# Optimization experiments

Measured on AMD Instinct MI355X. Metric: run time of the kernel, lower is better.

Reference implementation:

```python
import jax, jax.numpy as jnp
import numpy as np

N_PTS = 1_000_000
RES = 512
RANK = 48
OUT = 32
INIT_SCALE = 0.1


def _plane_sample(plane, gx, gy):
    """Bilinear grid_sample, align_corners=True, border padding.
    plane: [R, Res, Res] (R=rank); gx, gy: [N] in [-1,1] -> [R, N]."""
    res = plane.shape[-1]
    px = jnp.clip((gx + 1.0) * 0.5 * (res - 1), 0.0, res - 1.0)
    py = jnp.clip((gy + 1.0) * 0.5 * (res - 1), 0.0, res - 1.0)
    x0 = jnp.floor(px).astype(jnp.int32)
    y0 = jnp.floor(py).astype(jnp.int32)
    x1 = jnp.minimum(x0 + 1, res - 1)
    y1 = jnp.minimum(y0 + 1, res - 1)
    wx = px - x0.astype(px.dtype)
    wy = py - y0.astype(py.dtype)
    # gathers: [R, N] each
    v00 = plane[:, y0, x0]
    v01 = plane[:, y0, x1]
    v10 = plane[:, y1, x0]
    v11 = plane[:, y1, x1]
    return (v00 * (1 - wy) * (1 - wx) + v01 * (1 - wy) * wx
            + v10 * wy * (1 - wx) + v11 * wy * wx)


def _line_sample(line, gy):
    """Line is [R, Res] (width dim of size 1 collapses; x coord is 0 -> px=0).
    1-D linear interp along Res with gy in [-1,1] -> [R, N]."""
    res = line.shape[-1]
    py = jnp.clip((gy + 1.0) * 0.5 * (res - 1), 0.0, res - 1.0)
    y0 = jnp.floor(py).astype(jnp.int32)
    y1 = jnp.minimum(y0 + 1, res - 1)
    wy = py - y0.astype(py.dtype)
    return line[:, y0] * (1 - wy) + line[:, y1] * wy


def _geo_forward(coordinates, plane_xy, plane_xz, plane_yz,
                 line_z, line_y, line_x, proj_w, proj_b):
    coords = coordinates * 2.0 - 1.0  # [N, 3] in [-1, 1]
    cx, cy, cz = coords[:, 0], coords[:, 1], coords[:, 2]
    vm = (_plane_sample(plane_xy, cx, cy) * _line_sample(line_z, cz)
          + _plane_sample(plane_xz, cx, cz) * _line_sample(line_y, cy)
          + _plane_sample(plane_yz, cy, cz) * _line_sample(line_x, cx))  # [R, N]
    # projection: [N, R] @ [R, OUT] + b
    return vm.T @ proj_w.T + proj_b


def setup_inputs() -> dict:
    key = jax.random.key(0)
    ks = jax.random.split(key, 9)
    return {
        "coordinates": jax.random.uniform(ks[0], (N_PTS, 3), dtype=jnp.float32),
        "plane_xy": jax.random.normal(ks[1], (RANK, RES, RES), jnp.float32) * INIT_SCALE,
        "plane_xz": jax.random.normal(ks[2], (RANK, RES, RES), jnp.float32) * INIT_SCALE,
        "plane_yz": jax.random.normal(ks[3], (RANK, RES, RES), jnp.float32) * INIT_SCALE,
        "line_z": jax.random.normal(ks[4], (RANK, RES), jnp.float32) * INIT_SCALE,
        "line_y": jax.random.normal(ks[5], (RANK, RES), jnp.float32) * INIT_SCALE,
        "line_x": jax.random.normal(ks[6], (RANK, RES), jnp.float32) * INIT_SCALE,
        "proj_w": jax.random.normal(ks[7], (OUT, RANK), jnp.float32) * INIT_SCALE,
        "proj_b": jnp.zeros((OUT,), jnp.float32),
    }


def reference(coordinates, plane_xy, plane_xz, plane_yz,
              line_z, line_y, line_x, proj_w, proj_b):
    return _geo_forward(coordinates, plane_xy, plane_xz, plane_yz,
                        line_z, line_y, line_x, proj_w, proj_b)
```

## Files before the change

### kernel.cpp

```cpp
#include <hip/hip_runtime.h>
#include <stdint.h>

#define RES      512
#define TEXELS   (RES * RES)
#define NPTS     1000000
#define RANK     48
#define ODIM     32
#define PPB      64
#define VMS      52
#define OSTR     33
#define CELLS    32768
#define LINB     6
#define CNTB     256
#define TPB      1536
#define SCTB     1024

typedef unsigned int u32;
typedef float vf4 __attribute__((ext_vector_type(4)));

__device__ __forceinline__ float lobf(u32 u) { return __uint_as_float(u << 16); }
__device__ __forceinline__ float hibf(u32 u) { return __uint_as_float(u & 0xffff0000u); }

__device__ __forceinline__ float ntl(const float* p) {
    return __builtin_nontemporal_load(p);
}

__device__ __forceinline__ u32 pkbf(float a, float b) {
    u32 x = __float_as_uint(a), y = __float_as_uint(b);
    u32 xr = (x + 0x7fffu + ((x >> 16) & 1u)) >> 16;
    u32 yr = (y + 0x7fffu + ((y >> 16) & 1u)) & 0xffff0000u;
    return xr | yr;
}

__device__ __forceinline__ u32 sprd5(u32 a) {
    a &= 31u;
    a = (a | (a << 8)) & 0x100Fu;
    a = (a | (a << 4)) & 0x10C3u;
    a = (a | (a << 2)) & 0x1249u;
    return a;
}
__device__ __forceinline__ u32 cellOf(float x, float y, float z) {
    u32 cx = (u32)fminf(fmaxf(x * 32.f, 0.f), 31.f);
    u32 cy = (u32)fminf(fmaxf(y * 32.f, 0.f), 31.f);
    u32 cz = (u32)fminf(fmaxf(z * 32.f, 0.f), 31.f);
    return sprd5(cx) | (sprd5(cy) << 1) | (sprd5(cz) << 2);
}

__device__ __forceinline__ void tp_one(int g,
    const float* __restrict__ p0, const float* __restrict__ p1,
    const float* __restrict__ p2, char* __restrict__ ws)
{
    int plane = g >> 18;
    int texel = g & (TEXELS - 1);
    const float* src = (plane == 0) ? p0 : ((plane == 1) ? p1 : p2);
    u32 c2[24];
#pragma unroll
    for (int h = 0; h < 2; ++h) {
        float fa[12], fb[12];
#pragma unroll
        for (int d = 0; d < 12; ++d) {
            fa[d] = ntl(src + (size_t)(2 * (h * 12 + d) + 0) * TEXELS + texel);
            fb[d] = ntl(src + (size_t)(2 * (h * 12 + d) + 1) * TEXELS + texel);
        }
#pragma unroll
        for (int d = 0; d < 12; ++d) c2[h * 12 + d] = pkbf(fa[d], fb[d]);
    }
    char* dst = ws + (size_t)plane * TEXELS * 96 + (size_t)texel * 96;
#pragma unroll
    for (int s = 0; s < 6; ++s) {
        uint4 q = make_uint4(c2[4 * s + 0], c2[4 * s + 1],
                             c2[4 * s + 2], c2[4 * s + 3]);
        *(uint4*)(dst + 16 * s) = q;
    }
}

__device__ __forceinline__ void lines_role(int j, int t,
    const float* __restrict__ lz, const float* __restrict__ ly,
    const float* __restrict__ lx, char* __restrict__ ws)
{
    int id = j * 256 + t;
    int line = id >> 9;
    int pos = id & (RES - 1);
    const float* src = (line == 0) ? lz : ((line == 1) ? ly : lx);
    char* dst = ws + (size_t)3 * TEXELS * 96 + (size_t)line * RES * 96
                   + (size_t)pos * 96;
#pragma unroll
    for (int k = 0; k < 6; ++k) {
        uint4 q;
        q.x = pkbf(ntl(&src[(8 * k + 0) * RES + pos]), ntl(&src[(8 * k + 1) * RES + pos]));
        q.y = pkbf(ntl(&src[(8 * k + 2) * RES + pos]), ntl(&src[(8 * k + 3) * RES + pos]));
        q.z = pkbf(ntl(&src[(8 * k + 4) * RES + pos]), ntl(&src[(8 * k + 5) * RES + pos]));
        q.w = pkbf(ntl(&src[(8 * k + 6) * RES + pos]), ntl(&src[(8 * k + 7) * RES + pos]));
        *(uint4*)(dst + 16 * k) = q;
    }
}

__global__ __launch_bounds__(256) void k1_prep(
    const float* __restrict__ coords, u32* __restrict__ counts,
    const float* __restrict__ p0, const float* __restrict__ p1,
    const float* __restrict__ p2,
    const float* __restrict__ lz, const float* __restrict__ ly,
    const float* __restrict__ lx, char* __restrict__ ws)
{
    int bx = blockIdx.x, t = threadIdx.x;
    if (bx < LINB) {
        lines_role(bx, t, lz, ly, lx, ws);
    } else if (bx < LINB + CNTB) {
        for (int idx = (bx - LINB) * 256 + t; idx < NPTS; idx += CNTB * 256) {
            float x = ntl(&coords[3 * idx + 0]);
            float y = ntl(&coords[3 * idx + 1]);
            float z = ntl(&coords[3 * idx + 2]);
            atomicAdd(&counts[cellOf(x, y, z)], 1u);
        }
    } else {
        int w = bx - LINB - CNTB;
        for (int g = w * 256 + t; g < 3 * TEXELS; g += TPB * 256)
            tp_one(g, p0, p1, p2, ws);
    }
}

__global__ __launch_bounds__(1024) void k2_scan(
    const u32* __restrict__ counts, u32* __restrict__ cursors)
{
    __shared__ u32 wt[16];
    int t = threadIdx.x;
    u32 local[32];
    u32 s = 0;
#pragma unroll
    for (int i = 0; i < 32; ++i) {
        local[i] = s;
        s += counts[t * 32 + i];
    }
    u32 tot = s;
    int lane = t & 63, w = t >> 6;
    u32 incl = tot;
#pragma unroll
    for (int d = 1; d < 64; d <<= 1) {
        u32 v = __shfl_up(incl, d);
        if (lane >= d) incl += v;
    }
    if (lane == 63) wt[w] = incl;
    __syncthreads();
    if (t == 0) {
        u32 a = 0;
#pragma unroll
        for (int i = 0; i < 16; ++i) { u32 x = wt[i]; wt[i] = a; a += x; }
    }
    __syncthreads();
    u32 base = wt[w] + (incl - tot);
#pragma unroll
    for (int i = 0; i < 32; ++i)
        cursors[t * 32 + i] = base + local[i];
}

__global__ __launch_bounds__(256) void k3_scatter(
    const float* __restrict__ coords, u32* __restrict__ cursors,
    vf4* __restrict__ rc2)
{
    int t = threadIdx.x;
    for (int idx = blockIdx.x * 256 + t; idx < NPTS; idx += SCTB * 256) {
        float x = ntl(&coords[3 * idx + 0]);
        float y = ntl(&coords[3 * idx + 1]);
        float z = ntl(&coords[3 * idx + 2]);
        u32 pos = atomicAdd(&cursors[cellOf(x, y, z)], 1u);
        vf4 v; v.x = x; v.y = y; v.z = z; v.w = __uint_as_float((u32)idx);
        __builtin_nontemporal_store(v, rc2 + pos);
    }
}

__global__ __launch_bounds__(256) void tp_stream_only(
    const float* __restrict__ p0, const float* __restrict__ p1,
    const float* __restrict__ p2, char* __restrict__ ws)
{
    int g = blockIdx.x * 256 + threadIdx.x;
    tp_one(g, p0, p1, p2, ws);
}
__global__ __launch_bounds__(256) void lines_only(
    const float* __restrict__ lz, const float* __restrict__ ly,
    const float* __restrict__ lx, char* __restrict__ ws)
{
    lines_role(blockIdx.x, threadIdx.x, lz, ly, lx, ws);
}

__device__ __forceinline__ void prep1(float g, int& i0, int& i1, float& w) {
    float p = fminf(fmaxf((g + 1.f) * 0.5f * 511.f, 0.f), 511.f);
    float fp = floorf(p);
    i0 = (int)fp;
    i1 = min(i0 + 1, RES - 1);
    w = p - fp;
}

template <int TEXB, bool SORTED>
__global__ __launch_bounds__(512, 4) void geo_main(
    const void* __restrict__ cin, const char* __restrict__ ws,
    const float* __restrict__ W, const float* __restrict__ Bb,
    float* __restrict__ out)
{
    __shared__ float vm_lds[PPB * VMS];
    __shared__ u32 opt_lds[PPB];

    int tid = threadIdx.x;
    int ptL = tid >> 3;
    int c = tid & 7;

    int bid = blockIdx.x;
    if (SORTED) {
        int nwg = gridDim.x;
        int q = nwg >> 3, r = nwg & 7;
        int xcd = bid & 7, slot = bid >> 3;
        bid = (xcd < r ? xcd * (q + 1) : r * (q + 1) + (xcd - r) * q) + slot;
    }
    int pt = bid * PPB + ptL;

    float gx, gy, gz;
    if (SORTED) {
        vf4 cc = __builtin_nontemporal_load((const vf4*)cin + pt);
        gx = cc.x * 2.f - 1.f;
        gy = cc.y * 2.f - 1.f;
        gz = cc.z * 2.f - 1.f;
        if (c == 0) opt_lds[ptL] = __float_as_uint(cc.w);
    } else {
        const float* coords = (const float*)cin;
        gx = ntl(&coords[3 * pt + 0]) * 2.f - 1.f;
        gy = ntl(&coords[3 * pt + 1]) * 2.f - 1.f;
        gz = ntl(&coords[3 * pt + 2]) * 2.f - 1.f;
        if (c == 0) opt_lds[ptL] = (u32)pt;
    }

    int x0, x1, y0, y1, z0, z1;
    float wx, wy, wz;
    prep1(gx, x0, x1, wx);
    prep1(gy, y0, y1, wy);
    prep1(gz, z0, z1, wz);

    const size_t PW = (size_t)TEXELS * TEXB;
    const size_t LW = (size_t)RES * TEXB;
    const char* pxy = ws;
    const char* pxz = ws + PW;
    const char* pyz = ws + 2 * PW;
    const char* lzb = ws + 3 * PW;
    const char* lyb = lzb + LW;
    const char* lxb = lyb + LW;

    u32 co = 12u * (u32)c;

    u32 q[12][3], le[3][3], lf[3][3];
    {
        u32 offs[12];
        offs[0] = (u32)(y0 * RES + x0) * TEXB + co;
        offs[1] = (u32)(y0 * RES + x1) * TEXB + co;
        offs[2] = (u32)(y1 * RES + x0) * TEXB + co;
        offs[3] = (u32)(y1 * RES + x1) * TEXB + co;
        offs[4] = (u32)(z0 * RES + x0) * TEXB + co;
        offs[5] = (u32)(z0 * RES + x1) * TEXB + co;
        offs[6] = (u32)(z1 * RES + x0) * TEXB + co;
        offs[7] = (u32)(z1 * RES + x1) * TEXB + co;
        offs[8]  = (u32)(z0 * RES + y0) * TEXB + co;
        offs[9]  = (u32)(z0 * RES + y1) * TEXB + co;
        offs[10] = (u32)(z1 * RES + y0) * TEXB + co;
        offs[11] = (u32)(z1 * RES + y1) * TEXB + co;
        const char* bases[3] = { pxy, pxz, pyz };
#pragma unroll
        for (int p = 0; p < 3; ++p) {
#pragma unroll
            for (int k = 0; k < 4; ++k) {
                const u32* s = (const u32*)(bases[p] + offs[4 * p + k]);
                q[4 * p + k][0] = s[0];
                q[4 * p + k][1] = s[1];
                q[4 * p + k][2] = s[2];
            }
        }
        const char* lb[3] = { lzb, lyb, lxb };
        u32 l0[3] = { (u32)z0 * TEXB + co, (u32)y0 * TEXB + co, (u32)x0 * TEXB + co };
        u32 l1[3] = { (u32)z1 * TEXB + co, (u32)y1 * TEXB + co, (u32)x1 * TEXB + co };
#pragma unroll
        for (int p = 0; p < 3; ++p) {
            const u32* s0 = (const u32*)(lb[p] + l0[p]);
            const u32* s1 = (const u32*)(lb[p] + l1[p]);
            le[p][0] = s0[0]; le[p][1] = s0[1]; le[p][2] = s0[2];
            lf[p][0] = s1[0]; lf[p][1] = s1[1]; lf[p][2] = s1[2];
        }
    }

    float pw[3][4];
    pw[0][0] = (1.f - wy) * (1.f - wx); pw[0][1] = (1.f - wy) * wx;
    pw[0][2] = wy * (1.f - wx);         pw[0][3] = wy * wx;
    pw[1][0] = (1.f - wz) * (1.f - wx); pw[1][1] = (1.f - wz) * wx;
    pw[1][2] = wz * (1.f - wx);         pw[1][3] = wz * wx;
    pw[2][0] = (1.f - wz) * (1.f - wy); pw[2][1] = (1.f - wz) * wy;
    pw[2][2] = wz * (1.f - wy);         pw[2][3] = wz * wy;
    float lw[3] = { wz, wy, wx };

    float vm[6] = { 0.f, 0.f, 0.f, 0.f, 0.f, 0.f };
#pragma unroll
    for (int p = 0; p < 3; ++p) {
        float s0 = pw[p][0], s1 = pw[p][1], s2 = pw[p][2], s3 = pw[p][3];
        float il = 1.f - lw[p], wl = lw[p];
#pragma unroll
        for (int d = 0; d < 3; ++d) {
            u32 a = q[4 * p + 0][d], b = q[4 * p + 1][d];
            u32 cc = q[4 * p + 2][d], dd = q[4 * p + 3][d];
            float slo = s0 * lobf(a) + s1 * lobf(b) + s2 * lobf(cc) + s3 * lobf(dd);
            float shi = s0 * hibf(a) + s1 * hibf(b) + s2 * hibf(cc) + s3 * hibf(dd);
            float llo = il * lobf(le[p][d]) + wl * lobf(lf[p][d]);
            float lhi = il * hibf(le[p][d]) + wl * hibf(lf[p][d]);
            vm[2 * d + 0] = fmaf(slo, llo, vm[2 * d + 0]);
            vm[2 * d + 1] = fmaf(shi, lhi, vm[2 * d + 1]);
        }
    }

    float* vr = vm_lds + ptL * VMS + 6 * c;
    *(float2*)(vr + 0) = make_float2(vm[0], vm[1]);
    *(float2*)(vr + 2) = make_float2(vm[2], vm[3]);
    *(float2*)(vr + 4) = make_float2(vm[4], vm[5]);

    __syncthreads();

    int wav = __builtin_amdgcn_readfirstlane(tid >> 6);
    int lane = tid & 63;
    int ob = wav * 4;

    const float* vmrow = vm_lds + lane * VMS;
    float4 bb = *(const float4*)(Bb + ob);
    float a0 = bb.x, a1 = bb.y, a2 = bb.z, a3 = bb.w;
#pragma unroll 4
    for (int k = 0; k < 12; ++k) {
        float4 v = *(const float4*)(vmrow + 4 * k);
        float4 w0 = *(const float4*)(W + (ob + 0) * RANK + 4 * k);
        float4 w1 = *(const float4*)(W + (ob + 1) * RANK + 4 * k);
        float4 w2 = *(const float4*)(W + (ob + 2) * RANK + 4 * k);
        float4 w3 = *(const float4*)(W + (ob + 3) * RANK + 4 * k);
        a0 = fmaf(v.x, w0.x, a0); a0 = fmaf(v.y, w0.y, a0);
        a0 = fmaf(v.z, w0.z, a0); a0 = fmaf(v.w, w0.w, a0);
        a1 = fmaf(v.x, w1.x, a1); a1 = fmaf(v.y, w1.y, a1);
        a1 = fmaf(v.z, w1.z, a1); a1 = fmaf(v.w, w1.w, a1);
        a2 = fmaf(v.x, w2.x, a2); a2 = fmaf(v.y, w2.y, a2);
        a2 = fmaf(v.z, w2.z, a2); a2 = fmaf(v.w, w2.w, a2);
        a3 = fmaf(v.x, w3.x, a3); a3 = fmaf(v.y, w3.y, a3);
        a3 = fmaf(v.z, w3.z, a3); a3 = fmaf(v.w, w3.w, a3);
    }

    __syncthreads();
    {
        vf4 r; r.x = a0; r.y = a1; r.z = a2; r.w = a3;
        *(vf4*)(vm_lds + lane * OSTR + ob) = r;
    }
    __syncthreads();
    {
        int p8 = lane >> 3;
        int c2 = lane & 7;
        int gp = wav * 8 + p8;
        vf4 v = *(const vf4*)(vm_lds + gp * OSTR + 4 * c2);
        size_t orow = (size_t)opt_lds[gp];
        __builtin_nontemporal_store(v, (vf4*)(out + orow * ODIM + 4 * c2));
    }
}

extern "C" void kernel_launch(void* const* d_in, const int* in_sizes, int n_in,
                              void* d_out, int out_size, void* d_ws, size_t ws_size,
                              hipStream_t stream) {
    const float* coords = (const float*)d_in[0];
    const float* pxy = (const float*)d_in[1];
    const float* pxz = (const float*)d_in[2];
    const float* pyz = (const float*)d_in[3];
    const float* lz = (const float*)d_in[4];
    const float* ly = (const float*)d_in[5];
    const float* lx = (const float*)d_in[6];
    const float* W = (const float*)d_in[7];
    const float* Bb = (const float*)d_in[8];
    float* out = (float*)d_out;
    char* ws = (char*)d_ws;

    size_t pool96 = (size_t)3 * TEXELS * 96 + (size_t)3 * RES * 96;
    size_t o_counts = (pool96 + 255) & ~(size_t)255;
    size_t o_cursors = o_counts + (size_t)CELLS * 4;
    size_t o_rc2 = o_cursors + (size_t)CELLS * 4;
    size_t need_sorted = o_rc2 + (size_t)NPTS * 16;

    if (ws_size >= need_sorted) {
        u32* counts = (u32*)(ws + o_counts);
        u32* cursors = (u32*)(ws + o_cursors);
        vf4* rc2 = (vf4*)(ws + o_rc2);

        hipMemsetAsync(counts, 0, (size_t)CELLS * 4, stream);
        k1_prep<<<LINB + CNTB + TPB, 256, 0, stream>>>(coords, counts,
                                                       pxy, pxz, pyz,
                                                       lz, ly, lx, ws);
        k2_scan<<<1, 1024, 0, stream>>>(counts, cursors);
        k3_scatter<<<SCTB, 256, 0, stream>>>(coords, cursors, rc2);
        geo_main<96, true><<<NPTS / PPB, 512, 0, stream>>>(rc2, ws, W, Bb, out);
    } else {
        tp_stream_only<<<3 * TEXELS / 256, 256, 0, stream>>>(pxy, pxz, pyz, ws);
        lines_only<<<6, 256, 0, stream>>>(lz, ly, lx, ws);
        geo_main<96, false><<<NPTS / PPB, 512, 0, stream>>>(coords, ws, W, Bb, out);
    }
}
```

Baseline: 474.8 us.

## Use per-segment LDS histograms for binning and vectorize plane transpose

Replaces the global-atomic counting sort over a 32^3 Morton grid with a coarser 16^3 grid, where each of 256 segments builds a shared-memory histogram. A column-wise prefix over segments plus a base scan then lets the scatter kernel use LDS atomics. The memset and global atomic contention go away, and the scatter stays deterministic within each segment. The plane transpose now reads four texels per float4 load and writes four 96-byte records per thread. The coarser cells may reduce sampling locality in the main kernel.

```diff
diff --git a/kernel.cpp b/kernel.cpp
--- a/kernel.cpp
+++ b/kernel.cpp
@@ -9,11 +9,11 @@
 #define PPB      64
 #define VMS      52
 #define OSTR     33
-#define CELLS    32768
+#define NCELL    4096
+#define NSEG     256
+#define SEGSZ    3907
 #define LINB     6
-#define CNTB     256
-#define TPB      1536
-#define SCTB     1024
+#define TPB4     768
 
 typedef unsigned int u32;
 typedef float vf4 __attribute__((ext_vector_type(4)));
@@ -23,6 +23,9 @@
 
 __device__ __forceinline__ float ntl(const float* p) {
     return __builtin_nontemporal_load(p);
+}
+__device__ __forceinline__ vf4 ntl4(const float* p) {
+    return __builtin_nontemporal_load((const vf4*)p);
 }
 
 __device__ __forceinline__ u32 pkbf(float a, float b) {
@@ -32,45 +35,45 @@
     return xr | yr;
 }
 
-__device__ __forceinline__ u32 sprd5(u32 a) {
-    a &= 31u;
-    a = (a | (a << 8)) & 0x100Fu;
-    a = (a | (a << 4)) & 0x10C3u;
-    a = (a | (a << 2)) & 0x1249u;
+__device__ __forceinline__ u32 sprd4(u32 a) {
+    a &= 15u;
+    a = (a | (a << 4)) & 0x0C3u;
+    a = (a | (a << 2)) & 0x249u;
     return a;
 }
 __device__ __forceinline__ u32 cellOf(float x, float y, float z) {
-    u32 cx = (u32)fminf(fmaxf(x * 32.f, 0.f), 31.f);
-    u32 cy = (u32)fminf(fmaxf(y * 32.f, 0.f), 31.f);
-    u32 cz = (u32)fminf(fmaxf(z * 32.f, 0.f), 31.f);
-    return sprd5(cx) | (sprd5(cy) << 1) | (sprd5(cz) << 2);
-}
-
-__device__ __forceinline__ void tp_one(int g,
+    u32 cx = (u32)fminf(fmaxf(x * 16.f, 0.f), 15.f);
+    u32 cy = (u32)fminf(fmaxf(y * 16.f, 0.f), 15.f);
+    u32 cz = (u32)fminf(fmaxf(z * 16.f, 0.f), 15.f);
+    return sprd4(cx) | (sprd4(cy) << 1) | (sprd4(cz) << 2);
+}
+
+__device__ __forceinline__ void tp_one4(int g4,
     const float* __restrict__ p0, const float* __restrict__ p1,
     const float* __restrict__ p2, char* __restrict__ ws)
 {
-    int plane = g >> 18;
-    int texel = g & (TEXELS - 1);
+    int plane = g4 >> 16;
+    int t4 = g4 & (TEXELS / 4 - 1);
     const float* src = (plane == 0) ? p0 : ((plane == 1) ? p1 : p2);
-    u32 c2[24];
-#pragma unroll
-    for (int h = 0; h < 2; ++h) {
-        float fa[12], fb[12];
-#pragma unroll
-        for (int d = 0; d < 12; ++d) {
-            fa[d] = ntl(src + (size_t)(2 * (h * 12 + d) + 0) * TEXELS + texel);
-            fb[d] = ntl(src + (size_t)(2 * (h * 12 + d) + 1) * TEXELS + texel);
-        }
-#pragma unroll
-        for (int d = 0; d < 12; ++d) c2[h * 12 + d] = pkbf(fa[d], fb[d]);
-    }
-    char* dst = ws + (size_t)plane * TEXELS * 96 + (size_t)texel * 96;
+    int tex0 = t4 * 4;
+    char* dst = ws + (size_t)plane * TEXELS * 96 + (size_t)tex0 * 96;
 #pragma unroll
     for (int s = 0; s < 6; ++s) {
-        uint4 q = make_uint4(c2[4 * s + 0], c2[4 * s + 1],
-                             c2[4 * s + 2], c2[4 * s + 3]);
-        *(uint4*)(dst + 16 * s) = q;
+        vf4 fa[4], fb[4];
+#pragma unroll
+        for (int d = 0; d < 4; ++d) {
+            int dd = 4 * s + d;
+            fa[d] = ntl4(src + (size_t)(2 * dd + 0) * TEXELS + tex0);
+            fb[d] = ntl4(src + (size_t)(2 * dd + 1) * TEXELS + tex0);
+        }
+#pragma unroll
+        for (int k = 0; k < 4; ++k) {
+            uint4 q = make_uint4(pkbf(fa[0][k], fb[0][k]),
+                                 pkbf(fa[1][k], fb[1][k]),
+                                 pkbf(fa[2][k], fb[2][k]),
+                                 pkbf(fa[3][k], fb[3][k]));
+            *(uint4*)(dst + (size_t)k * 96 + 16 * s) = q;
+        }
     }
 }
 
@@ -96,41 +99,65 @@
 }
 
 __global__ __launch_bounds__(256) void k1_prep(
-    const float* __restrict__ coords, u32* __restrict__ counts,
+    const float* __restrict__ coords, u32* __restrict__ T,
     const float* __restrict__ p0, const float* __restrict__ p1,
     const float* __restrict__ p2,
     const float* __restrict__ lz, const float* __restrict__ ly,
     const float* __restrict__ lx, char* __restrict__ ws)
 {
+    __shared__ u32 hist[NCELL];
     int bx = blockIdx.x, t = threadIdx.x;
     if (bx < LINB) {
         lines_role(bx, t, lz, ly, lx, ws);
-    } else if (bx < LINB + CNTB) {
-        for (int idx = (bx - LINB) * 256 + t; idx < NPTS; idx += CNTB * 256) {
+    } else if (bx < LINB + NSEG) {
+        int s = bx - LINB;
+#pragma unroll
+        for (int i = 0; i < NCELL / 256; ++i) hist[t + 256 * i] = 0u;
+        __syncthreads();
+        int base = s * SEGSZ;
+        int lim = min(base + SEGSZ, NPTS);
+#pragma unroll 1
+        for (int idx = base + t; idx < lim; idx += 256) {
             float x = ntl(&coords[3 * idx + 0]);
             float y = ntl(&coords[3 * idx + 1]);
             float z = ntl(&coords[3 * idx + 2]);
-            atomicAdd(&counts[cellOf(x, y, z)], 1u);
+            atomicAdd(&hist[cellOf(x, y, z)], 1u);
+        }
+        __syncthreads();
+        u32* Ts = T + (size_t)s * NCELL;
+#pragma unroll
+        for (int i = 0; i < NCELL / 256; ++i) {
+            int cc = t + 256 * i;
+            Ts[cc] = hist[cc];
         }
     } else {
-        int w = bx - LINB - CNTB;
-        for (int g = w * 256 + t; g < 3 * TEXELS; g += TPB * 256)
-            tp_one(g, p0, p1, p2, ws);
-    }
-}
-
-__global__ __launch_bounds__(1024) void k2_scan(
-    const u32* __restrict__ counts, u32* __restrict__ cursors)
-{
-    __shared__ u32 wt[16];
+        tp_one4((bx - LINB - NSEG) * 256 + t, p0, p1, p2, ws);
+    }
+}
+
+__global__ __launch_bounds__(256) void k2_prefix(
+    u32* __restrict__ T, u32* __restrict__ cellTot)
+{
+    int c = blockIdx.x * 256 + threadIdx.x;
+    u32 run = 0;
+#pragma unroll 8
+    for (int s = 0; s < NSEG; ++s) {
+        u32 v = T[(size_t)s * NCELL + c];
+        T[(size_t)s * NCELL + c] = run;
+        run += v;
+    }
+    cellTot[c] = run;
+}
+
+__global__ __launch_bounds__(256) void k2_base(
+    const u32* __restrict__ cellTot, u32* __restrict__ cellBase)
+{
+    __shared__ u32 wt[4];
     int t = threadIdx.x;
-    u32 local[32];
+    u32 loc[16];
     u32 s = 0;
 #pragma unroll
-    for (int i = 0; i < 32; ++i) {
-        local[i] = s;
-        s += counts[t * 32 + i];
-    }
+    for (int i = 0; i < 16; ++i) { loc[i] = s; s += cellTot[t * 16 + i]; }
     u32 tot = s;
     int lane = t & 63, w = t >> 6;
     u32 incl = tot;
@@ -141,28 +168,34 @@
     }
     if (lane == 63) wt[w] = incl;
     __syncthreads();
-    if (t == 0) {
-        u32 a = 0;
-#pragma unroll
-        for (int i = 0; i < 16; ++i) { u32 x = wt[i]; wt[i] = a; a += x; }
+    u32 base = incl - tot;
+#pragma unroll
+    for (int i = 0; i < 4; ++i) base += (i < w) ? wt[i] : 0u;
+#pragma unroll
+    for (int i = 0; i < 16; ++i) cellBase[t * 16 + i] = base + loc[i];
+}
+
+__global__ __launch_bounds__(256) void k3_scatter(
+    const float* __restrict__ coords, const u32* __restrict__ T,
+    const u32* __restrict__ cellBase, vf4* __restrict__ rc2)
+{
+    __shared__ u32 cur[NCELL];
+    int s = blockIdx.x, t = threadIdx.x;
+    const u32* Ts = T + (size_t)s * NCELL;
+#pragma unroll
+    for (int i = 0; i < NCELL / 256; ++i) {
+        int cc = t + 256 * i;
+        cur[cc] = cellBase[cc] + Ts[cc];
     }
     __syncthreads();
-    u32 base = wt[w] + (incl - tot);
-#pragma unroll
-    for (int i = 0; i < 32; ++i)
-        cursors[t * 32 + i] = base + local[i];
-}
-
-__global__ __launch_bounds__(256) void k3_scatter(
-    const float* __restrict__ coords, u32* __restrict__ cursors,
-    vf4* __restrict__ rc2)
-{
-    int t = threadIdx.x;
-    for (int idx = blockIdx.x * 256 + t; idx < NPTS; idx += SCTB * 256) {
+    int base = s * SEGSZ;
+    int lim = min(base + SEGSZ, NPTS);
+#pragma unroll 1
+    for (int idx = base + t; idx < lim; idx += 256) {
         float x = ntl(&coords[3 * idx + 0]);
         float y = ntl(&coords[3 * idx + 1]);
         float z = ntl(&coords[3 * idx + 2]);
-        u32 pos = atomicAdd(&cursors[cellOf(x, y, z)], 1u);
+        u32 pos = atomicAdd(&cur[cellOf(x, y, z)], 1u);
         vf4 v; v.x = x; v.y = y; v.z = z; v.w = __uint_as_float((u32)idx);
         __builtin_nontemporal_store(v, rc2 + pos);
     }
@@ -172,8 +205,7 @@
     const float* __restrict__ p0, const float* __restrict__ p1,
     const float* __restrict__ p2, char* __restrict__ ws)
 {
-    int g = blockIdx.x * 256 + threadIdx.x;
-    tp_one(g, p0, p1, p2, ws);
+    tp_one4(blockIdx.x * 256 + threadIdx.x, p0, p1, p2, ws);
 }
 __global__ __launch_bounds__(256) void lines_only(
     const float* __restrict__ lz, const float* __restrict__ ly,
@@ -372,25 +404,27 @@
     char* ws = (char*)d_ws;
 
     size_t pool96 = (size_t)3 * TEXELS * 96 + (size_t)3 * RES * 96;
-    size_t o_counts = (pool96 + 255) & ~(size_t)255;
-    size_t o_cursors = o_counts + (size_t)CELLS * 4;
-    size_t o_rc2 = o_cursors + (size_t)CELLS * 4;
+    size_t o_T = (pool96 + 255) & ~(size_t)255;
+    size_t o_ct = o_T + (size_t)NSEG * NCELL * 4;
+    size_t o_cb = o_ct + (size_t)NCELL * 4;
+    size_t o_rc2 = o_cb + (size_t)NCELL * 4;
     size_t need_sorted = o_rc2 + (size_t)NPTS * 16;
 
     if (ws_size >= need_sorted) {
-        u32* counts = (u32*)(ws + o_counts);
-        u32* cursors = (u32*)(ws + o_cursors);
+        u32* T = (u32*)(ws + o_T);
+        u32* cellTot = (u32*)(ws + o_ct);
+        u32* cellBase = (u32*)(ws + o_cb);
         vf4* rc2 = (vf4*)(ws + o_rc2);
 
-        hipMemsetAsync(counts, 0, (size_t)CELLS * 4, stream);
-        k1_prep<<<LINB + CNTB + TPB, 256, 0, stream>>>(coords, counts,
-                                                       pxy, pxz, pyz,
-                                                       lz, ly, lx, ws);
-        k2_scan<<<1, 1024, 0, stream>>>(counts, cursors);
-        k3_scatter<<<SCTB, 256, 0, stream>>>(coords, cursors, rc2);
+        k1_prep<<<LINB + NSEG + TPB4, 256, 0, stream>>>(coords, T,
+                                                        pxy, pxz, pyz,
+                                                        lz, ly, lx, ws);
+        k2_prefix<<<NCELL / 256, 256, 0, stream>>>(T, cellTot);
+        k2_base<<<1, 256, 0, stream>>>(cellTot, cellBase);
+        k3_scatter<<<NSEG, 256, 0, stream>>>(coords, T, cellBase, rc2);
         geo_main<96, true><<<NPTS / PPB, 512, 0, stream>>>(rc2, ws, W, Bb, out);
     } else {
-        tp_stream_only<<<3 * TEXELS / 256, 256, 0, stream>>>(pxy, pxz, pyz, ws);
+        tp_stream_only<<<TPB4, 256, 0, stream>>>(pxy, pxz, pyz, ws);
         lines_only<<<6, 256, 0, stream>>>(lz, ly, lx, ws);
         geo_main<96, false><<<NPTS / PPB, 512, 0, stream>>>(coords, ws, W, Bb, out);
     }
```

Measured after the change: 466.2 us. Within noise of the previous version (-1.8%).
